# Performance work log

Hardware: AMD Instinct MI355X
Metric: run time of the kernel (lower is better)

Reference implementation:

```python
import jax, jax.numpy as jnp
import numpy as np

B, PRE, POST = 32, 2048, 2048
TAU_PRE = 2.0
TAU_POST = 2.0
V_TH = 1.0  # IF-neuron firing threshold


def setup_inputs() -> dict:
    key = jax.random.key(0)
    k1, k2, k3, k4 = jax.random.split(key, 4)
    # input spikes are binary (Bernoulli p=0.2)
    x = (jax.random.uniform(k1, (B, PRE)) < 0.2).astype(jnp.float32)
    # Linear weight [post, pre], Kaiming-ish scale
    W = jax.random.normal(k2, (POST, PRE), dtype=jnp.float32) / np.sqrt(PRE)
    # pre/post traces carried over from previous timesteps
    trace_pre = jax.random.uniform(k3, (B, PRE), dtype=jnp.float32)
    trace_post = jax.random.uniform(k4, (B, POST), dtype=jnp.float32)
    return {"x": x, "W": W, "trace_pre": trace_pre, "trace_post": trace_post}


def reference(x, W, trace_pre, trace_post):
    # connection: i = x @ W^T  -> [B, POST]
    i = x @ W.T
    # node: IF neuron, Heaviside spike
    spike = (i >= V_TH).astype(x.dtype)
    # trace decay (EMA) + spike accumulation
    tp = trace_pre - trace_pre / TAU_PRE + x        # [B, PRE]
    tq = trace_post - trace_post / TAU_POST + spike  # [B, POST]
    # clamp weight once; batch outer-product sums expressed as GEMMs
    Wc = jnp.clip(W, -1.0, 1.0)
    dw = (-Wc * jnp.einsum('bp,bq->pq', tq, x)
          + Wc * jnp.einsum('bp,bq->pq', spike, tp))  # [POST, PRE]
    return (spike, dw)
```

## Files before the change

### kernel.cpp

```cpp
#include <hip/hip_runtime.h>

#define B_ 32
#define PRE_ 2048
#define POST_ 2048
#define QT 4
#define WPAD 2056

#define XROW_OFF 0
#define FRAG_OFF 65536
#define SPQ_OFF  196608

typedef __attribute__((ext_vector_type(8))) short short8;
typedef __attribute__((ext_vector_type(4))) short short4v;
typedef __attribute__((ext_vector_type(4))) float floatx4;

__device__ __forceinline__ unsigned short f2bf(float f) {
    unsigned u = __float_as_uint(f);
    u += 0x7FFF + ((u >> 16) & 1);
    return (unsigned short)(u >> 16);
}
__device__ __forceinline__ float bf2f(unsigned short h) {
    return __uint_as_float(((unsigned)h) << 16);
}

__global__ __launch_bounds__(64) void stdp_prep(
    const float* __restrict__ x, const float* __restrict__ tpre,
    unsigned short* __restrict__ ws)
{
    __shared__ __align__(16) unsigned short tt[8 * 80];
    const int lane = threadIdx.x;
    const int p0 = blockIdx.x * 8;
    const int b = lane >> 1, c4 = (lane & 1) * 4;

    floatx4 xv = *(const floatx4*)(x    + b * PRE_ + p0 + c4);
    floatx4 tv = *(const floatx4*)(tpre + b * PRE_ + p0 + c4);
    short4v xr;
#pragma unroll
    for (int j = 0; j < 4; ++j) {
        xr[j] = (short)(__float_as_uint(xv[j]) >> 16);
        tt[(c4 + j) * 80 + b]      = f2bf(0.5f * tv[j] + xv[j]);
        tt[(c4 + j) * 80 + 32 + b] = (unsigned short)xr[j];
    }
    *(short4v*)(ws + XROW_OFF + b * PRE_ + p0 + c4) = xr;
    __syncthreads();
    const int pp = lane >> 3, seg = lane & 7;
    short8 v = *(const short8*)(tt + pp * 80 + seg * 8);
    *(short8*)(ws + FRAG_OFF + (p0 + pp) * 64 + seg * 8) = v;
}

__global__ __launch_bounds__(512) void stdp_fwd(
    const float* __restrict__ W, const float* __restrict__ tpost,
    unsigned short* __restrict__ ws, float* __restrict__ out)
{
    __shared__ __align__(16) unsigned short sh[2 * QT * WPAD];
    unsigned short* Wh = sh;
    unsigned short* Wl = sh + QT * WPAD;
    float* red = (float*)sh;

    const int tid  = threadIdx.x;
    const int wave = tid >> 6, lane = tid & 63;
    const int quad = lane >> 4, l16 = lane & 15;
    const int q0   = blockIdx.x * QT;
    const int qb   = l16 & (QT - 1);
    const int kbase = wave * 256;

    float tpr[4];
    if (wave < 2 && l16 < QT) {
#pragma unroll
        for (int r = 0; r < 4; ++r)
            tpr[r] = tpost[(wave * 16 + quad * 4 + r) * POST_ + q0 + l16];
    }

    floatx4 wv[QT];
#pragma unroll
    for (int r = 0; r < QT; ++r)
        wv[r] = *(const floatx4*)(W + (q0 + r) * PRE_ + kbase + lane * 4);
#pragma unroll
    for (int r = 0; r < QT; ++r) {
        short4v hv, lv;
#pragma unroll
        for (int j = 0; j < 4; ++j) {
            unsigned short h = f2bf(wv[r][j]);
            hv[j] = (short)h;
            lv[j] = (short)f2bf(wv[r][j] - bf2f(h));
        }
        *(short4v*)&Wh[r * WPAD + kbase + lane * 4] = hv;
        *(short4v*)&Wl[r * WPAD + kbase + lane * 4] = lv;
    }

    const unsigned short* xrow = ws + XROW_OFF;
    floatx4 acc0 = {0.f, 0.f, 0.f, 0.f};
    floatx4 acc1 = {0.f, 0.f, 0.f, 0.f};
#pragma unroll
    for (int s = 0; s < 8; ++s) {
        int ko = kbase + s * 32 + quad * 8;
        short8 a0 = *(const short8*)(xrow + l16 * PRE_ + ko);
        short8 a1 = *(const short8*)(xrow + (16 + l16) * PRE_ + ko);
        short8 bh = *(const short8*)(Wh + qb * WPAD + ko);
        short8 bl = *(const short8*)(Wl + qb * WPAD + ko);
        acc0 = __builtin_amdgcn_mfma_f32_16x16x32_bf16(a0, bh, acc0, 0, 0, 0);
        acc0 = __builtin_amdgcn_mfma_f32_16x16x32_bf16(a0, bl, acc0, 0, 0, 0);
        acc1 = __builtin_amdgcn_mfma_f32_16x16x32_bf16(a1, bh, acc1, 0, 0, 0);
        acc1 = __builtin_amdgcn_mfma_f32_16x16x32_bf16(a1, bl, acc1, 0, 0, 0);
    }

    __syncthreads();
#pragma unroll
    for (int r = 0; r < 4; ++r) {
        red[((wave * 2 + 0) * 4 + r) * 64 + lane] = acc0[r];
        red[((wave * 2 + 1) * 4 + r) * 64 + lane] = acc1[r];
    }
    __syncthreads();

    if (wave < 2 && l16 < QT) {
        unsigned short* spq = ws + SPQ_OFF;
        int q = q0 + l16;
#pragma unroll
        for (int r = 0; r < 4; ++r) {
            float s = 0.f;
#pragma unroll
            for (int w = 0; w < 8; ++w) s += red[((w * 2 + wave) * 4 + r) * 64 + lane];
            int b = wave * 16 + quad * 4 + r;
            float spike = (s >= 1.0f) ? 1.0f : 0.0f;
            out[b * POST_ + q] = spike;
            float ntq = -(0.5f * tpr[r] + spike);
            spq[q * 64 + b]      = f2bf(spike);
            spq[q * 64 + 32 + b] = f2bf(ntq);
        }
    }
}

__global__ __launch_bounds__(256) void stdp_dw(
    const float* __restrict__ W, const unsigned short* __restrict__ ws,
    float* __restrict__ out)
{
    const unsigned short* frag = ws + FRAG_OFF;
    const unsigned short* spq  = ws + SPQ_OFF;
    float* dw = out + B_ * POST_;

    const int tid  = threadIdx.x;
    const int wave = tid >> 6, lane = tid & 63;
    const int quad = lane >> 4, l16 = lane & 15;
    const int wid = (blockIdx.x & 7) * 128 + (blockIdx.x >> 3);
    const int gw  = wid * 4 + wave;
    const int qt  = gw >> 5;
    const int ps  = gw & 31;
    const int q   = qt * 16 + l16;
    const int p0  = ps * 64;

    short8 fsp = *(const short8*)(spq + q * 64 + quad * 8);
    short8 fnq = *(const short8*)(spq + q * 64 + 32 + quad * 8);

#pragma unroll
    for (int it = 0; it < 4; ++it) {
        int p = p0 + it * 16;
        short8 ftp = *(const short8*)(frag + (p + l16) * 64 + quad * 8);
        short8 fx  = *(const short8*)(frag + (p + l16) * 64 + 32 + quad * 8);
        floatx4 acc = {0.f, 0.f, 0.f, 0.f};
        acc = __builtin_amdgcn_mfma_f32_16x16x32_bf16(ftp, fsp, acc, 0, 0, 0);
        acc = __builtin_amdgcn_mfma_f32_16x16x32_bf16(fx,  fnq, acc, 0, 0, 0);
        floatx4 wq = *(const floatx4*)(W + q * PRE_ + p + quad * 4);
        floatx4 o;
#pragma unroll
        for (int r = 0; r < 4; ++r) {
            float wc = fminf(fmaxf(wq[r], -1.0f), 1.0f);
            o[r] = wc * acc[r];
        }
        *(floatx4*)(dw + q * PRE_ + p + quad * 4) = o;
    }
}

extern "C" void kernel_launch(void* const* d_in, const int* in_sizes, int n_in,
                              void* d_out, int out_size, void* d_ws, size_t ws_size,
                              hipStream_t stream) {
    const float* x     = (const float*)d_in[0];
    const float* W     = (const float*)d_in[1];
    const float* tpre  = (const float*)d_in[2];
    const float* tpost = (const float*)d_in[3];
    float* out = (float*)d_out;
    unsigned short* ws = (unsigned short*)d_ws;

    hipLaunchKernelGGL(stdp_prep, dim3(256), dim3(64), 0, stream, x, tpre, ws);
    hipLaunchKernelGGL(stdp_fwd,  dim3(POST_ / QT), dim3(512), 0, stream,
                       W, tpost, ws, out);
    hipLaunchKernelGGL(stdp_dw,   dim3(1024), dim3(256), 0, stream, W, ws, out);
}
```

Before: 96.88 us.

## Fuse prep kernel into forward kernel, reading fp32 spikes directly

Removes the separate stdp_prep launch. The forward kernel now reads x as fp32 and truncates it to bf16 in registers instead of loading a bf16 copy from workspace. One partial wave per block also builds the pre-trace/x fragment buffer for the dw kernel. This saves a kernel launch and one round trip through the workspace. In exchange, the forward kernel reads twice the bytes for x and does extra conversion work, and the fragment stores are scalar and uncoalesced.

```diff
diff --git a/kernel.cpp b/kernel.cpp
--- a/kernel.cpp
+++ b/kernel.cpp
@@ -6,7 +6,6 @@
 #define QT 4
 #define WPAD 2056
 
-#define XROW_OFF 0
 #define FRAG_OFF 65536
 #define SPQ_OFF  196608
 
@@ -23,33 +22,9 @@
     return __uint_as_float(((unsigned)h) << 16);
 }
 
-__global__ __launch_bounds__(64) void stdp_prep(
-    const float* __restrict__ x, const float* __restrict__ tpre,
-    unsigned short* __restrict__ ws)
-{
-    __shared__ __align__(16) unsigned short tt[8 * 80];
-    const int lane = threadIdx.x;
-    const int p0 = blockIdx.x * 8;
-    const int b = lane >> 1, c4 = (lane & 1) * 4;
-
-    floatx4 xv = *(const floatx4*)(x    + b * PRE_ + p0 + c4);
-    floatx4 tv = *(const floatx4*)(tpre + b * PRE_ + p0 + c4);
-    short4v xr;
-#pragma unroll
-    for (int j = 0; j < 4; ++j) {
-        xr[j] = (short)(__float_as_uint(xv[j]) >> 16);
-        tt[(c4 + j) * 80 + b]      = f2bf(0.5f * tv[j] + xv[j]);
-        tt[(c4 + j) * 80 + 32 + b] = (unsigned short)xr[j];
-    }
-    *(short4v*)(ws + XROW_OFF + b * PRE_ + p0 + c4) = xr;
-    __syncthreads();
-    const int pp = lane >> 3, seg = lane & 7;
-    short8 v = *(const short8*)(tt + pp * 80 + seg * 8);
-    *(short8*)(ws + FRAG_OFF + (p0 + pp) * 64 + seg * 8) = v;
-}
-
 __global__ __launch_bounds__(512) void stdp_fwd(
-    const float* __restrict__ W, const float* __restrict__ tpost,
+    const float* __restrict__ W, const float* __restrict__ x,
+    const float* __restrict__ tpre, const float* __restrict__ tpost,
     unsigned short* __restrict__ ws, float* __restrict__ out)
 {
     __shared__ __align__(16) unsigned short sh[2 * QT * WPAD];
@@ -63,6 +38,19 @@
     const int q0   = blockIdx.x * QT;
     const int qb   = l16 & (QT - 1);
     const int kbase = wave * 256;
+
+    if (wave == 7 && lane < 32) {
+        const int p0 = blockIdx.x * 4;
+        unsigned short* frag = ws + FRAG_OFF;
+        floatx4 xv = *(const floatx4*)(x    + lane * PRE_ + p0);
+        floatx4 tv = *(const floatx4*)(tpre + lane * PRE_ + p0);
+#pragma unroll
+        for (int c = 0; c < 4; ++c) {
+            frag[(p0 + c) * 64 + lane]      = f2bf(0.5f * tv[c] + xv[c]);
+            frag[(p0 + c) * 64 + 32 + lane] =
+                (unsigned short)(__float_as_uint(xv[c]) >> 16);
+        }
+    }
 
     float tpr[4];
     if (wave < 2 && l16 < QT) {
@@ -88,14 +76,23 @@
         *(short4v*)&Wl[r * WPAD + kbase + lane * 4] = lv;
     }
 
-    const unsigned short* xrow = ws + XROW_OFF;
     floatx4 acc0 = {0.f, 0.f, 0.f, 0.f};
     floatx4 acc1 = {0.f, 0.f, 0.f, 0.f};
 #pragma unroll
     for (int s = 0; s < 8; ++s) {
         int ko = kbase + s * 32 + quad * 8;
-        short8 a0 = *(const short8*)(xrow + l16 * PRE_ + ko);
-        short8 a1 = *(const short8*)(xrow + (16 + l16) * PRE_ + ko);
+        floatx4 xa0 = *(const floatx4*)(x + l16 * PRE_ + ko);
+        floatx4 xa1 = *(const floatx4*)(x + l16 * PRE_ + ko + 4);
+        floatx4 xb0 = *(const floatx4*)(x + (16 + l16) * PRE_ + ko);
+        floatx4 xb1 = *(const floatx4*)(x + (16 + l16) * PRE_ + ko + 4);
+        short8 a0, a1;
+#pragma unroll
+        for (int j = 0; j < 4; ++j) {
+            a0[j]     = (short)(__float_as_uint(xa0[j]) >> 16);
+            a0[4 + j] = (short)(__float_as_uint(xa1[j]) >> 16);
+            a1[j]     = (short)(__float_as_uint(xb0[j]) >> 16);
+            a1[4 + j] = (short)(__float_as_uint(xb1[j]) >> 16);
+        }
         short8 bh = *(const short8*)(Wh + qb * WPAD + ko);
         short8 bl = *(const short8*)(Wl + qb * WPAD + ko);
         acc0 = __builtin_amdgcn_mfma_f32_16x16x32_bf16(a0, bh, acc0, 0, 0, 0);
@@ -180,8 +177,7 @@
     float* out = (float*)d_out;
     unsigned short* ws = (unsigned short*)d_ws;
 
-    hipLaunchKernelGGL(stdp_prep, dim3(256), dim3(64), 0, stream, x, tpre, ws);
-    hipLaunchKernelGGL(stdp_fwd,  dim3(POST_ / QT), dim3(512), 0, stream,
-                       W, tpost, ws, out);
-    hipLaunchKernelGGL(stdp_dw,   dim3(1024), dim3(256), 0, stream, W, ws, out);
+    hipLaunchKernelGGL(stdp_fwd, dim3(POST_ / QT), dim3(512), 0, stream,
+                       W, x, tpre, tpost, ws, out);
+    hipLaunchKernelGGL(stdp_dw,  dim3(1024), dim3(256), 0, stream, W, ws, out);
 }
```

Result: slower. 103.0 us (+6.3%).
